# Optimization experiments

Hardware: AMD Instinct MI355X
Metric: run time of the kernel (lower is better)

Reference implementation:

```python
import jax, jax.numpy as jnp
import numpy as np

B, LQ, LK, DQ, DKEY, DV = 8, 2048, 2048, 1024, 1024, 1024
MASK_NEG = -1e6  # d2l masked_softmax fill value


def setup_inputs() -> dict:
    key = jax.random.key(0)
    kq, kk, kv, kl, kw = jax.random.split(key, 5)
    queries = jax.random.normal(kq, (B, LQ, DQ), dtype=jnp.float32)
    keys = jax.random.normal(kk, (B, LK, DKEY), dtype=jnp.float32)
    values = jax.random.normal(kv, (B, LK, DV), dtype=jnp.float32)
    valid_lens = jax.random.randint(kl, (B,), 1, LK + 1)
    W_q = jax.random.normal(kw, (DQ, DKEY), dtype=jnp.float32) / np.sqrt(DQ)
    return {"queries": queries, "keys": keys, "values": values,
            "valid_lens": valid_lens, "W_q": W_q}


def reference(queries, keys, values, valid_lens, W_q):
    # Q projection: LazyLinear(key_dim, bias=False)
    q = jnp.einsum("bqd,dk->bqk", queries, W_q)          # [B, LQ, DKEY]
    d = q.shape[-1]
    scores = jnp.einsum("bqk,bsk->bqs", q, keys) / jnp.sqrt(jnp.asarray(d, q.dtype))
    # masked_softmax: positions >= valid_len set to -1e6 before softmax
    mask = jnp.arange(scores.shape[-1])[None, None, :] < valid_lens[:, None, None]
    scores = jnp.where(mask, scores, MASK_NEG)
    attn = jax.nn.softmax(scores, axis=-1)               # [B, LQ, LK]
    # dropout p=0.0 (eval) -> identity
    return jnp.einsum("bqs,bsv->bqv", attn, values)      # [B, LQ, DV]
```

## Files before the change

### kernel.cpp

```cpp
#include <hip/hip_runtime.h>
#include <cstdint>
#include <cstddef>

#define B_   8
#define LQ_  2048
#define LK_  2048

typedef __attribute__((ext_vector_type(8))) __bf16 bf16x8;
typedef __attribute__((ext_vector_type(4))) float f32x4;
typedef __attribute__((ext_vector_type(8))) unsigned short ushortx8;

__device__ __forceinline__ unsigned short f2bf(float f) {
  unsigned u = __builtin_bit_cast(unsigned, f);
  u = u + 0x7fffu + ((u >> 16) & 1u);
  return (unsigned short)(u >> 16);
}
__device__ __forceinline__ float bf2f(unsigned short h) {
  unsigned u = ((unsigned)h) << 16;
  return __builtin_bit_cast(float, u);
}

__device__ __forceinline__ void gld_lds16(const void* g, void* l) {
  __builtin_amdgcn_global_load_lds((__attribute__((address_space(1))) void*)(void*)g,
                                   (__attribute__((address_space(3))) void*)l, 16, 0, 0);
}

__global__ __launch_bounds__(256) void cast3_bf16_kernel(
    const float* __restrict__ q, unsigned short* __restrict__ qo,
    const float* __restrict__ k, unsigned short* __restrict__ ko,
    const float* __restrict__ w, unsigned short* __restrict__ wo,
    const int* __restrict__ vlp) {
  int bb = (int)blockIdx.x;
  const float* in;
  unsigned short* out;
  if (bb < 8192) {
    in = q; out = qo;
  } else if (bb < 16384) {
    bb -= 8192;
    in = k; out = ko;
    int batch = bb >> 10;
    int row = (bb & 1023) * 2;
    int vl = vlp[batch];
    if (row >= ((vl + 255) & ~255)) return;
  } else {
    bb -= 16384;
    in = w; out = wo;
  }
  size_t i = ((size_t)bb * 256 + threadIdx.x) * 8;
  float4 a = *(const float4*)(in + i);
  float4 b = *(const float4*)(in + i + 4);
  ushortx8 o;
  o[0] = f2bf(a.x); o[1] = f2bf(a.y); o[2] = f2bf(a.z); o[3] = f2bf(a.w);
  o[4] = f2bf(b.x); o[5] = f2bf(b.y); o[6] = f2bf(b.z); o[7] = f2bf(b.w);
  *(ushortx8*)(out + i) = o;
}

__global__ __launch_bounds__(256) void transpose_cast_kernel(
    const float* __restrict__ in, unsigned short* __restrict__ out,
    int R, int C, long in_bstride, long out_bstride, const int* __restrict__ vlp) {
  __shared__ float t[32][33];
  int r0 = blockIdx.y * 32;
  if (vlp) {
    int kEnd = (vlp[blockIdx.z] + 63) & ~63;
    if (r0 >= kEnd) return;
  }
  const float* inb = in + (size_t)blockIdx.z * in_bstride;
  unsigned short* outb = out + (size_t)blockIdx.z * out_bstride;
  int c0 = blockIdx.x * 32;
  int tx = threadIdx.x, ty = threadIdx.y;
#pragma unroll
  for (int k = 0; k < 4; ++k) {
    int r = ty + k * 8;
    t[r][tx] = inb[(size_t)(r0 + r) * C + c0 + tx];
  }
  __syncthreads();
#pragma unroll
  for (int k = 0; k < 4; ++k) {
    int c = ty + k * 8;
    outb[(size_t)(c0 + c) * R + r0 + tx] = f2bf(t[tx][c]);
  }
}

template <int OUTM, int SKIPN, int SKIPM, int CLAMPK>
__global__ __launch_bounds__(256, 2) void gemm256x128_kernel(
    const unsigned short* __restrict__ A, const unsigned short* __restrict__ B,
    void* __restrict__ Cp, int M, int N, int K,
    long a_bstride, long b_bstride, long c_bstride, float scale,
    const int* __restrict__ vlp, int lognx) {
  __shared__ unsigned short lds[3][128 * 64 + 64 * 64];

  const int tid = threadIdx.x;
  const int wid = tid >> 6;
  const int lane = tid & 63;
  const int lane15 = lane & 15;
  const int lhalf = lane >> 4;

  const int idx = (int)blockIdx.x;
  const int z = idx & 7;
  const int rest = idx >> 3;
  const int nxm = (1 << lognx) - 1;
  const int xt = rest & nxm;
  const int yt = rest >> lognx;
  const int nt = (xt + 2 * z) & nxm;
  const int m0 = yt * 256;
  const int n0 = nt * 128;

  int vl = K;
  if constexpr (SKIPN || SKIPM || CLAMPK) vl = vlp[z];
  if constexpr (SKIPN) {
    if (n0 >= vl) return;
  }
  if constexpr (SKIPM) {
    if (m0 >= vl) return;
  }
  int kEnd = K;
  if constexpr (CLAMPK) {
    int ke = (vl + 63) & ~63;
    kEnd = ke < K ? ke : K;
  }
  const int nKt = kEnd >> 5;

  const unsigned short* Ab = A + (size_t)z * a_bstride;
  const unsigned short* Bb = B + (size_t)z * b_bstride;

  int srA[4], scA[4], sdA[4];
#pragma unroll
  for (int j = 0; j < 4; ++j) {
    int blk = (wid * 4 + j) * 64 + lane;
    int p = blk >> 3;
    int c = (blk & 7) ^ (p & 7);
    srA[j] = m0 + 2 * p + (c >> 2);
    scA[j] = (c & 3) * 8;
    sdA[j] = blk * 8;
  }
  int srB[2], scB[2], sdB[2];
#pragma unroll
  for (int j = 0; j < 2; ++j) {
    int blk = (wid * 2 + j) * 64 + lane;
    int p = blk >> 3;
    int c = (blk & 7) ^ (p & 7);
    srB[j] = n0 + 2 * p + (c >> 2);
    scB[j] = (c & 3) * 8;
    sdB[j] = 8192 + blk * 8;
  }

  const int om = (wid & 1) * 128;
  const int on = (wid >> 1) * 64;
  const int swz8 = ((((lane15 & 1) << 2) + lhalf) ^ ((lane15 >> 1) & 7)) << 3;
  const int aBase = ((om >> 1) + (lane15 >> 1)) * 64 + swz8;
  const int bBase = 8192 + ((on >> 1) + (lane15 >> 1)) * 64 + swz8;

  f32x4 acc[8][4];
#pragma unroll
  for (int f = 0; f < 8; ++f)
#pragma unroll
    for (int g = 0; g < 4; ++g) acc[f][g] = (f32x4){0.f, 0.f, 0.f, 0.f};

#define STAGE_TILE(T, S)                                                        \
  {                                                                             \
    const int kc_ = (T) * 32;                                                   \
    _Pragma("unroll")                                                           \
    for (int j = 0; j < 4; ++j)                                                 \
      gld_lds16(Ab + (size_t)srA[j] * K + (kc_ + scA[j]), &lds[S][sdA[j]]);     \
    _Pragma("unroll")                                                           \
    for (int j = 0; j < 2; ++j)                                                 \
      gld_lds16(Bb + (size_t)srB[j] * K + (kc_ + scB[j]), &lds[S][sdB[j]]);     \
  }

  STAGE_TILE(0, 0);
  STAGE_TILE(1, 1);
  asm volatile("s_waitcnt vmcnt(6)" ::: "memory");
  __builtin_amdgcn_s_barrier();

  int cs = 0;
  for (int t = 0; t < nKt; ++t) {
    const unsigned short* lcur = &lds[cs][0];
    const bool st = (t + 2) < nKt;
    const int ss = cs == 0 ? 2 : cs - 1;

    bf16x8 a[8], b[4];
#pragma unroll
    for (int f = 0; f < 8; ++f) a[f] = *(const bf16x8*)&lcur[aBase + f * 512];
#pragma unroll
    for (int g = 0; g < 4; ++g) b[g] = *(const bf16x8*)&lcur[bBase + g * 512];
    if (st) STAGE_TILE(t + 2, ss);
    asm volatile("s_waitcnt lgkmcnt(0)" ::: "memory");
    __builtin_amdgcn_sched_barrier(0);
    __builtin_amdgcn_s_setprio(1);
#pragma unroll
    for (int f = 0; f < 8; ++f)
#pragma unroll
      for (int g = 0; g < 4; ++g)
        acc[f][g] = __builtin_amdgcn_mfma_f32_16x16x32_bf16(a[f], b[g], acc[f][g], 0, 0, 0);
    __builtin_amdgcn_s_setprio(0);
    if (st)
      asm volatile("s_waitcnt vmcnt(6)" ::: "memory");
    else
      asm volatile("s_waitcnt vmcnt(0)" ::: "memory");
    __builtin_amdgcn_s_barrier();
    cs = cs == 2 ? 0 : cs + 1;
  }
#undef STAGE_TILE

  const size_t boffC = (size_t)z * c_bstride;
#pragma unroll
  for (int f = 0; f < 8; ++f) {
    int row = m0 + om + f * 16 + lhalf * 4;
#pragma unroll
    for (int g = 0; g < 4; ++g) {
      int col = n0 + on + g * 16 + lane15;
#pragma unroll
      for (int r = 0; r < 4; ++r) {
        float v = acc[f][g][r];
        if constexpr (OUTM == 0) {
          ((unsigned short*)Cp + boffC)[(size_t)(row + r) * N + col] = f2bf(v);
        } else if constexpr (OUTM == 1) {
          ((unsigned short*)Cp + boffC)[(size_t)(row + r) * N + col] = f2bf(v * scale);
        } else {
          ((float*)Cp + boffC)[(size_t)(row + r) * N + col] = v;
        }
      }
    }
  }
}

__global__ __launch_bounds__(256) void softmax_kernel(unsigned short* __restrict__ scores,
                                                      const int* __restrict__ valid_lens) {
  const int row = blockIdx.x;
  const int b = row >> 11;
  const int vl = valid_lens[b];
  const int kEnd = (vl + 63) & ~63;
  unsigned short* rp = scores + (size_t)row * LK_;
  const int tid = threadIdx.x;
  const int wid = tid >> 6, lane = tid & 63;
  __shared__ float sred[4];

  const int cb = tid * 8;
  const bool act = cb < kEnd;
  ushortx8 h = {};
  if (act) h = *(const ushortx8*)(rp + cb);
  float x[8];
#pragma unroll
  for (int t = 0; t < 8; ++t) x[t] = bf2f(h[t]);

  float m = -3.4e38f;
#pragma unroll
  for (int t = 0; t < 8; ++t)
    if (cb + t < vl) m = fmaxf(m, x[t]);
#pragma unroll
  for (int off = 32; off >= 1; off >>= 1) m = fmaxf(m, __shfl_xor(m, off));
  if (lane == 0) sred[wid] = m;
  __syncthreads();
  m = fmaxf(fmaxf(sred[0], sred[1]), fmaxf(sred[2], sred[3]));
  __syncthreads();

  float e[8];
  float s = 0.f;
#pragma unroll
  for (int t = 0; t < 8; ++t) {
    e[t] = (cb + t < vl) ? __expf(x[t] - m) : 0.f;
    s += e[t];
  }
#pragma unroll
  for (int off = 32; off >= 1; off >>= 1) s += __shfl_xor(s, off);
  if (lane == 0) sred[wid] = s;
  __syncthreads();
  s = sred[0] + sred[1] + sred[2] + sred[3];
  float inv = 1.f / s;

  if (act) {
    ushortx8 o;
#pragma unroll
    for (int t = 0; t < 8; ++t) o[t] = f2bf(e[t] * inv);
    *(ushortx8*)(rp + cb) = o;
  }
}

extern "C" void kernel_launch(void* const* d_in, const int* in_sizes, int n_in,
                              void* d_out, int out_size, void* d_ws, size_t ws_size,
                              hipStream_t stream) {
  const float* queries = (const float*)d_in[0];
  const float* keys = (const float*)d_in[1];
  const float* values = (const float*)d_in[2];
  const int* valid_lens = (const int*)d_in[3];
  const float* W_q = (const float*)d_in[4];
  float* out = (float*)d_out;

  unsigned short* ws = (unsigned short*)d_ws;
  const size_t M1 = (size_t)1024 * 1024;
  unsigned short* q_bf = ws;
  unsigned short* scores = ws + 16 * M1;
  unsigned short* keysP = ws + 48 * M1;
  unsigned short* valsT = keysP;
  unsigned short* w_bf = ws + 64 * M1;
  unsigned short* keys_bf = ws + 65 * M1;

  cast3_bf16_kernel<<<dim3(16896), 256, 0, stream>>>(
      queries, q_bf, keys, keys_bf, W_q, w_bf, valid_lens);
  gemm256x128_kernel<0, 0, 1, 0><<<dim3(8 * 8 * 8), 256, 0, stream>>>(
      keys_bf, w_bf, keysP, 2048, 1024, 1024,
      (long)2048 * 1024, 0, (long)2048 * 1024, 1.f, valid_lens, 3);
  gemm256x128_kernel<1, 1, 0, 0><<<dim3(8 * 16 * 8), 256, 0, stream>>>(
      q_bf, keysP, scores, 2048, 2048, 1024,
      (long)2048 * 1024, (long)2048 * 1024, (long)2048 * 2048, 0.03125f, valid_lens, 4);
  transpose_cast_kernel<<<dim3(32, 64, 8), dim3(32, 8), 0, stream>>>(
      values, valsT, 2048, 1024, (long)2048 * 1024, (long)1024 * 2048, valid_lens);
  softmax_kernel<<<dim3(B_ * LQ_), 256, 0, stream>>>(scores, valid_lens);
  gemm256x128_kernel<2, 0, 0, 1><<<dim3(8 * 8 * 8), 256, 0, stream>>>(
      scores, valsT, out, 2048, 1024, 2048,
      (long)2048 * 2048, (long)1024 * 2048, (long)2048 * 1024, 1.f, valid_lens, 3);
}
```

Measured before the change: 374.8 us.

## Double-buffer GEMM LDS for three blocks per CU; merge transpose and softmax launches

The GEMM drops from a three-stage to a two-stage LDS ring (about 48KB to 32KB) and raises the launch bound to three blocks per CU. The aim is more occupancy to hide latency. In exchange, the prefetch depth shrinks to one tile and every iteration now waits on vmcnt(0). Separately, the V transpose-cast kernel and the softmax kernel are merged into one launch that picks its role from the block index, removing a launch and letting the two independent jobs overlap.

```diff
diff --git a/kernel.cpp b/kernel.cpp
--- a/kernel.cpp
+++ b/kernel.cpp
@@ -55,39 +55,13 @@
   *(ushortx8*)(out + i) = o;
 }
 
-__global__ __launch_bounds__(256) void transpose_cast_kernel(
-    const float* __restrict__ in, unsigned short* __restrict__ out,
-    int R, int C, long in_bstride, long out_bstride, const int* __restrict__ vlp) {
-  __shared__ float t[32][33];
-  int r0 = blockIdx.y * 32;
-  if (vlp) {
-    int kEnd = (vlp[blockIdx.z] + 63) & ~63;
-    if (r0 >= kEnd) return;
-  }
-  const float* inb = in + (size_t)blockIdx.z * in_bstride;
-  unsigned short* outb = out + (size_t)blockIdx.z * out_bstride;
-  int c0 = blockIdx.x * 32;
-  int tx = threadIdx.x, ty = threadIdx.y;
-#pragma unroll
-  for (int k = 0; k < 4; ++k) {
-    int r = ty + k * 8;
-    t[r][tx] = inb[(size_t)(r0 + r) * C + c0 + tx];
-  }
-  __syncthreads();
-#pragma unroll
-  for (int k = 0; k < 4; ++k) {
-    int c = ty + k * 8;
-    outb[(size_t)(c0 + c) * R + r0 + tx] = f2bf(t[tx][c]);
-  }
-}
-
 template <int OUTM, int SKIPN, int SKIPM, int CLAMPK>
-__global__ __launch_bounds__(256, 2) void gemm256x128_kernel(
+__global__ __launch_bounds__(256, 3) void gemm256x128_kernel(
     const unsigned short* __restrict__ A, const unsigned short* __restrict__ B,
     void* __restrict__ Cp, int M, int N, int K,
     long a_bstride, long b_bstride, long c_bstride, float scale,
     const int* __restrict__ vlp, int lognx) {
-  __shared__ unsigned short lds[3][128 * 64 + 64 * 64];
+  __shared__ unsigned short lds[2][128 * 64 + 64 * 64];
 
   const int tid = threadIdx.x;
   const int wid = tid >> 6;
@@ -168,22 +142,18 @@
   }
 
   STAGE_TILE(0, 0);
-  STAGE_TILE(1, 1);
-  asm volatile("s_waitcnt vmcnt(6)" ::: "memory");
+  asm volatile("s_waitcnt vmcnt(0)" ::: "memory");
   __builtin_amdgcn_s_barrier();
 
-  int cs = 0;
   for (int t = 0; t < nKt; ++t) {
-    const unsigned short* lcur = &lds[cs][0];
-    const bool st = (t + 2) < nKt;
-    const int ss = cs == 0 ? 2 : cs - 1;
+    const unsigned short* lcur = &lds[t & 1][0];
+    if (t + 1 < nKt) STAGE_TILE(t + 1, (t + 1) & 1);
 
     bf16x8 a[8], b[4];
 #pragma unroll
     for (int f = 0; f < 8; ++f) a[f] = *(const bf16x8*)&lcur[aBase + f * 512];
 #pragma unroll
     for (int g = 0; g < 4; ++g) b[g] = *(const bf16x8*)&lcur[bBase + g * 512];
-    if (st) STAGE_TILE(t + 2, ss);
     asm volatile("s_waitcnt lgkmcnt(0)" ::: "memory");
     __builtin_amdgcn_sched_barrier(0);
     __builtin_amdgcn_s_setprio(1);
@@ -193,12 +163,8 @@
       for (int g = 0; g < 4; ++g)
         acc[f][g] = __builtin_amdgcn_mfma_f32_16x16x32_bf16(a[f], b[g], acc[f][g], 0, 0, 0);
     __builtin_amdgcn_s_setprio(0);
-    if (st)
-      asm volatile("s_waitcnt vmcnt(6)" ::: "memory");
-    else
-      asm volatile("s_waitcnt vmcnt(0)" ::: "memory");
+    asm volatile("s_waitcnt vmcnt(0)" ::: "memory");
     __builtin_amdgcn_s_barrier();
-    cs = cs == 2 ? 0 : cs + 1;
   }
 #undef STAGE_TILE
 
@@ -224,16 +190,43 @@
   }
 }
 
-__global__ __launch_bounds__(256) void softmax_kernel(unsigned short* __restrict__ scores,
-                                                      const int* __restrict__ valid_lens) {
-  const int row = blockIdx.x;
+__global__ __launch_bounds__(256) void vtrans_softmax_kernel(
+    const float* __restrict__ vals, unsigned short* __restrict__ valsT,
+    unsigned short* __restrict__ scores, const int* __restrict__ valid_lens) {
+  __shared__ float smem[32 * 33];
+  const int bb = (int)blockIdx.x;
+  const int tid = threadIdx.x;
+
+  if (bb < 16384) {
+    const int z = bb >> 11;
+    const int r0 = ((bb >> 5) & 63) * 32;
+    const int kEnd = (valid_lens[z] + 63) & ~63;
+    if (r0 >= kEnd) return;
+    const int c0 = (bb & 31) * 32;
+    const int tx = tid & 31, ty = tid >> 5;
+    const float* inb = vals + (size_t)z * 2048 * 1024;
+    unsigned short* outb = valsT + (size_t)z * 1024 * 2048;
+#pragma unroll
+    for (int k = 0; k < 4; ++k) {
+      int r = ty + k * 8;
+      smem[r * 33 + tx] = inb[(size_t)(r0 + r) * 1024 + c0 + tx];
+    }
+    __syncthreads();
+#pragma unroll
+    for (int k = 0; k < 4; ++k) {
+      int c = ty + k * 8;
+      outb[(size_t)(c0 + c) * 2048 + r0 + tx] = f2bf(smem[tx * 33 + c]);
+    }
+    return;
+  }
+
+  const int row = bb - 16384;
   const int b = row >> 11;
   const int vl = valid_lens[b];
   const int kEnd = (vl + 63) & ~63;
   unsigned short* rp = scores + (size_t)row * LK_;
-  const int tid = threadIdx.x;
   const int wid = tid >> 6, lane = tid & 63;
-  __shared__ float sred[4];
+  float* sred = smem;
 
   const int cb = tid * 8;
   const bool act = cb < kEnd;
@@ -303,9 +296,8 @@
   gemm256x128_kernel<1, 1, 0, 0><<<dim3(8 * 16 * 8), 256, 0, stream>>>(
       q_bf, keysP, scores, 2048, 2048, 1024,
       (long)2048 * 1024, (long)2048 * 1024, (long)2048 * 2048, 0.03125f, valid_lens, 4);
-  transpose_cast_kernel<<<dim3(32, 64, 8), dim3(32, 8), 0, stream>>>(
-      values, valsT, 2048, 1024, (long)2048 * 1024, (long)1024 * 2048, valid_lens);
-  softmax_kernel<<<dim3(B_ * LQ_), 256, 0, stream>>>(scores, valid_lens);
+  vtrans_softmax_kernel<<<dim3(32768), 256, 0, stream>>>(
+      values, valsT, scores, valid_lens);
   gemm256x128_kernel<2, 0, 0, 1><<<dim3(8 * 8 * 8), 256, 0, stream>>>(
       scores, valsT, out, 2048, 1024, 2048,
       (long)2048 * 2048, (long)1024 * 2048, (long)2048 * 1024, 1.f, valid_lens, 3);
```

Result: slower. 862.3 us (+130.1%).
